# Performance work log

Measured on AMD Instinct MI355X. Metric: run time of the kernel, lower is better.

The kernel has to match this reference:

```python
import jax, jax.numpy as jnp
import numpy as np

D_MODEL = 1024
N_HEADS = 16
HEAD_DIM = D_MODEL // N_HEADS
NEG = -10000.0  # module uses -10000, not -inf


def setup_inputs() -> dict:
    key = jax.random.key(0)
    ks = jax.random.split(key, 8)
    B, T = 4, 2048
    q = jax.random.normal(ks[0], (B, T, D_MODEL), dtype=jnp.float32)
    k = jax.random.normal(ks[1], (B, T, D_MODEL), dtype=jnp.float32)
    v = jax.random.normal(ks[2], (B, T, D_MODEL), dtype=jnp.float32)
    attn_mask = jnp.ones((B, T), dtype=jnp.float32)
    # xavier_uniform for square [d, d] weights: limit = sqrt(6/(d+d))
    lim = float(np.sqrt(6.0 / (D_MODEL + D_MODEL)))
    Wq = jax.random.uniform(ks[3], (D_MODEL, D_MODEL), jnp.float32, -lim, lim)
    Wk = jax.random.uniform(ks[4], (D_MODEL, D_MODEL), jnp.float32, -lim, lim)
    Wv = jax.random.uniform(ks[5], (D_MODEL, D_MODEL), jnp.float32, -lim, lim)
    Wo = jax.random.uniform(ks[6], (D_MODEL, D_MODEL), jnp.float32, -lim, lim)
    return {"q": q, "k": k, "v": v, "attn_mask": attn_mask,
            "Wq": Wq, "Wk": Wk, "Wv": Wv, "Wo": Wo, "mask_future": 1}


def _split_heads(x):
    B, T, _ = x.shape
    return x.reshape(B, T, N_HEADS, HEAD_DIM).transpose(0, 2, 1, 3)  # [B,H,T,D]


def reference(q, k, v, attn_mask, Wq, Wk, Wv, Wo, mask_future):
    # torch Linear: y = x @ W.T  (weights stored [out, in])
    qh = _split_heads(jnp.einsum('btd,ed->bte', q, Wq))
    kh = _split_heads(jnp.einsum('btd,ed->bte', k, Wk))
    vh = _split_heads(jnp.einsum('btd,ed->bte', v, Wv))
    L, S = qh.shape[-2], kh.shape[-2]
    # dual scale: each of q and k scaled by 1/d**0.25
    scale = 1.0 / jnp.sqrt(jnp.sqrt(jnp.float32(HEAD_DIM)))
    scores = jnp.einsum('bhld,bhsd->bhls', qh * scale, kh * scale)
    if mask_future:
        causal_bias = jnp.triu(jnp.full((L, S), NEG, dtype=scores.dtype), k=1)
        scores = scores + causal_bias
    # padding mask: attn_mask [B, S] -> broadcast [B,1,1,S]; 0 entries -> -10000
    pad = attn_mask[:, None, None, :]
    scores = jnp.where(pad == 0, jnp.asarray(NEG, scores.dtype), scores)
    probs = jax.nn.softmax(scores, axis=-1)  # dropout p=0.0 -> identity
    ctx = jnp.einsum('bhls,bhsd->bhld', probs, vh)
    B = ctx.shape[0]
    ctx = ctx.transpose(0, 2, 1, 3).reshape(B, L, D_MODEL)
    return jnp.einsum('btd,ed->bte', ctx, Wo)
```

## Files before the change

kernel.cpp:

```cpp
#include <hip/hip_runtime.h>

typedef unsigned short u16;
typedef __attribute__((ext_vector_type(8))) _Float16 f16x8;
typedef __attribute__((ext_vector_type(2))) __fp16 fp16v2;
typedef __attribute__((ext_vector_type(4))) float f32x4;
typedef __attribute__((ext_vector_type(16))) float f32x16;

#define T_SEQ 2048
#define NH 16
#define DH 64
#define DM 1024
#define NEG2 (-14426.95f)
#define QS2 (0.42466089f)

__device__ __forceinline__ unsigned pk2(float a, float b) {
  union { fp16v2 v; unsigned u; } c;
  c.v = __builtin_amdgcn_cvt_pkrtz(a, b);
  return c.u;
}
__device__ __forceinline__ u16 f2h(float a) {
  union { _Float16 h; u16 u; } c; c.h = (_Float16)a; return c.u;
}

__device__ __forceinline__ void async_load16(const void* g, void* l) {
  __builtin_amdgcn_global_load_lds(
      (const __attribute__((address_space(1))) unsigned int*)(g),
      (__attribute__((address_space(3))) unsigned int*)(l), 16, 0, 0);
}

__global__ __launch_bounds__(256) void convert_all(
    const float* __restrict__ q, const float* __restrict__ k, const float* __restrict__ v,
    const float* __restrict__ Wq, const float* __restrict__ Wk, const float* __restrict__ Wv,
    const float* __restrict__ Wo, u16* __restrict__ xb, u16* __restrict__ wb) {
  int blk = blockIdx.x;
  const float* src; u16* dst;
  if (blk < 12288) {
    int s = blk >> 12;
    src = (s == 0) ? q : (s == 1) ? k : v;
    dst = xb + (size_t)s * 8388608u;
    blk &= 4095;
  } else {
    int s = (blk - 12288) >> 9;
    src = (s == 0) ? Wq : (s == 1) ? Wk : (s == 2) ? Wv : Wo;
    dst = wb + (size_t)s * 1048576u;
    blk = (blk - 12288) & 511;
  }
  size_t base = (size_t)blk * 2048 + (size_t)threadIdx.x * 8;
  float4 a = *(const float4*)(src + base);
  float4 b2 = *(const float4*)(src + base + 4);
  uint4 st;
  st.x = pk2(a.x, a.y); st.y = pk2(a.z, a.w);
  st.z = pk2(b2.x, b2.y); st.w = pk2(b2.z, b2.w);
  *(uint4*)(dst + base) = st;
}

__global__ __launch_bounds__(256) void gemm_qkv(const u16* __restrict__ A,
                                                const u16* __restrict__ Wqb,
                                                const u16* __restrict__ Wkb,
                                                const u16* __restrict__ Wvb,
                                                u16* __restrict__ Qh, u16* __restrict__ Kh,
                                                u16* __restrict__ VTh) {
  __shared__ char lds[49152];
  const int tid = threadIdx.x;
  const int wid = tid >> 6, lane = tid & 63;
  const int l32 = lane & 31, lh = lane >> 5;
  const int m0 = blockIdx.x * 128;
  const int n0 = blockIdx.y * 128;
  const int which = n0 >> 10;
  const int n0l = n0 & 1023;
  const u16* As = A + (size_t)which * 8388608u;
  const u16* Bw = (which == 0) ? Wqb : (which == 1) ? Wkb : Wvb;
  const int wm = wid >> 1, wn = wid & 1;
  f32x16 acc[2][2] = {};

  const u16* gA = As + (size_t)(m0 + wid * 32 + l32) * 1024 + lh * 8;
  const u16* gB = Bw + (size_t)(n0l + wid * 32 + l32) * 1024 + lh * 8;
  for (int t = 0; t < 2; ++t) {
    char* bf = lds + t * 16384;
    async_load16(gA + t * 32, bf + (wid * 2 + 0) * 1024);
    async_load16(gA + t * 32 + 16, bf + (wid * 2 + 1) * 1024);
    async_load16(gB + t * 32, bf + 8192 + (wid * 2 + 0) * 1024);
    async_load16(gB + t * 32 + 16, bf + 8192 + (wid * 2 + 1) * 1024);
  }

  int buf = 0;
  for (int it = 0; it < 32; ++it) {
    if (it < 31) asm volatile("s_waitcnt vmcnt(4)" ::: "memory");
    else         asm volatile("s_waitcnt vmcnt(0)" ::: "memory");
    __builtin_amdgcn_s_barrier();
    asm volatile("" ::: "memory");
    char* cur = lds + buf * 16384;
    if (it < 30) {
      char* nxt = lds + ((buf == 0) ? 2 : buf - 1) * 16384;
      int kt = (it + 2) * 32;
      async_load16(gA + kt, nxt + (wid * 2 + 0) * 1024);
      async_load16(gA + kt + 16, nxt + (wid * 2 + 1) * 1024);
      async_load16(gB + kt, nxt + 8192 + (wid * 2 + 0) * 1024);
      async_load16(gB + kt + 16, nxt + 8192 + (wid * 2 + 1) * 1024);
    }
    char* const rb = (which < 2) ? (cur + 8192) : cur;
    char* const cb = (which < 2) ? cur : (cur + 8192);
    f16x8 rf0[2], cf0[2], rf1[2], cf1[2];
    for (int i = 0; i < 2; ++i) {
      rf0[i] = *(const f16x8*)(rb + ((wm * 2 + i) * 2 + 0) * 1024 + lane * 16);
      cf0[i] = *(const f16x8*)(cb + ((wn * 2 + i) * 2 + 0) * 1024 + lane * 16);
    }
    for (int i = 0; i < 2; ++i) {
      rf1[i] = *(const f16x8*)(rb + ((wm * 2 + i) * 2 + 1) * 1024 + lane * 16);
      cf1[i] = *(const f16x8*)(cb + ((wn * 2 + i) * 2 + 1) * 1024 + lane * 16);
    }
    for (int i = 0; i < 2; ++i)
      for (int j = 0; j < 2; ++j)
        acc[i][j] = __builtin_amdgcn_mfma_f32_32x32x16_f16(rf0[i], cf0[j], acc[i][j], 0, 0, 0);
    for (int i = 0; i < 2; ++i)
      for (int j = 0; j < 2; ++j)
        acc[i][j] = __builtin_amdgcn_mfma_f32_32x32x16_f16(rf1[i], cf1[j], acc[i][j], 0, 0, 0);
    buf = (buf == 2) ? 0 : buf + 1;
  }

  const float s = (which < 2) ? QS2 : 1.0f;
  __syncthreads();
  for (int i = 0; i < 2; ++i)
    for (int j = 0; j < 2; ++j) {
      int colb = wn * 64 + j * 32 + l32;
      int rowb = wm * 64 + i * 32 + 4 * lh;
      for (int g = 0; g < 4; ++g) {
        uint2 pv;
        pv.x = pk2(acc[i][j][4 * g + 0] * s, acc[i][j][4 * g + 1] * s);
        pv.y = pk2(acc[i][j][4 * g + 2] * s, acc[i][j][4 * g + 3] * s);
        *(uint2*)(lds + colb * 264 + (rowb + 8 * g) * 2) = pv;
      }
    }
  __syncthreads();

  const int b = m0 >> 11, t0 = m0 & 2047, h0 = n0l >> 6;
  if (which < 2) {
    u16* O = which ? Kh : Qh;
    for (int p = 0; p < 8; ++p) {
      int row = p * 16 + (tid >> 4);
      int seg = tid & 15;
      uint4 val = *(const uint4*)(lds + row * 264 + seg * 16);
      int hl = seg >> 3, dh0 = (seg & 7) * 8;
      *(uint4*)(O + (((size_t)(b * NH + h0 + hl) * T_SEQ + t0 + row) << 6) + dh0) = val;
    }
  } else {
    for (int p = 0; p < 8; ++p) {
      int row = p * 16 + (tid >> 4);
      int seg = tid & 15;
      uint4 val = *(const uint4*)(lds + row * 264 + seg * 16);
      int h = h0 + (row >> 6), dh = row & 63;
      *(uint4*)(VTh + (((size_t)(b * NH + h) * DH + dh) << 11) + t0 + seg * 8) = val;
    }
  }
}

__global__ __launch_bounds__(256) void gemm_out(const u16* __restrict__ A,
                                                const u16* __restrict__ Bw,
                                                float* __restrict__ O) {
  __shared__ char lds[49152];
  const int tid = threadIdx.x;
  const int wid = tid >> 6, lane = tid & 63;
  const int l32 = lane & 31, lh = lane >> 5;
  const int m0 = blockIdx.x * 128, n0 = blockIdx.y * 128;
  const int wm = wid >> 1, wn = wid & 1;
  f32x16 acc[2][2] = {};

  const u16* gA = A + (size_t)(m0 + wid * 32 + l32) * 1024 + lh * 8;
  const u16* gB = Bw + (size_t)(n0 + wid * 32 + l32) * 1024 + lh * 8;
  for (int t = 0; t < 2; ++t) {
    char* bf = lds + t * 16384;
    async_load16(gA + t * 32, bf + (wid * 2 + 0) * 1024);
    async_load16(gA + t * 32 + 16, bf + (wid * 2 + 1) * 1024);
    async_load16(gB + t * 32, bf + 8192 + (wid * 2 + 0) * 1024);
    async_load16(gB + t * 32 + 16, bf + 8192 + (wid * 2 + 1) * 1024);
  }

  int buf = 0;
  for (int it = 0; it < 32; ++it) {
    if (it < 31) asm volatile("s_waitcnt vmcnt(4)" ::: "memory");
    else         asm volatile("s_waitcnt vmcnt(0)" ::: "memory");
    __builtin_amdgcn_s_barrier();
    asm volatile("" ::: "memory");
    char* cur = lds + buf * 16384;
    if (it < 30) {
      char* nxt = lds + ((buf == 0) ? 2 : buf - 1) * 16384;
      int kt = (it + 2) * 32;
      async_load16(gA + kt, nxt + (wid * 2 + 0) * 1024);
      async_load16(gA + kt + 16, nxt + (wid * 2 + 1) * 1024);
      async_load16(gB + kt, nxt + 8192 + (wid * 2 + 0) * 1024);
      async_load16(gB + kt + 16, nxt + 8192 + (wid * 2 + 1) * 1024);
    }
    f16x8 af0[2], bf0[2], af1[2], bf1[2];
    for (int i = 0; i < 2; ++i) {
      af0[i] = *(const f16x8*)(cur + ((wm * 2 + i) * 2 + 0) * 1024 + lane * 16);
      bf0[i] = *(const f16x8*)(cur + 8192 + ((wn * 2 + i) * 2 + 0) * 1024 + lane * 16);
    }
    for (int i = 0; i < 2; ++i) {
      af1[i] = *(const f16x8*)(cur + ((wm * 2 + i) * 2 + 1) * 1024 + lane * 16);
      bf1[i] = *(const f16x8*)(cur + 8192 + ((wn * 2 + i) * 2 + 1) * 1024 + lane * 16);
    }
    for (int i = 0; i < 2; ++i)
      for (int j = 0; j < 2; ++j)
        acc[i][j] = __builtin_amdgcn_mfma_f32_32x32x16_f16(af0[i], bf0[j], acc[i][j], 0, 0, 0);
    for (int i = 0; i < 2; ++i)
      for (int j = 0; j < 2; ++j)
        acc[i][j] = __builtin_amdgcn_mfma_f32_32x32x16_f16(af1[i], bf1[j], acc[i][j], 0, 0, 0);
    buf = (buf == 2) ? 0 : buf + 1;
  }
  for (int i = 0; i < 2; ++i)
    for (int j = 0; j < 2; ++j) {
      int col = n0 + wn * 64 + j * 32 + l32;
      int rowb = m0 + wm * 64 + i * 32 + 4 * lh;
      for (int g = 0; g < 4; ++g)
        for (int rr = 0; rr < 4; ++rr)
          O[(size_t)(rowb + 8 * g + rr) * 1024 + col] = acc[i][j][4 * g + rr];
    }
}

__global__ __launch_bounds__(512) void attn_kernel(const u16* __restrict__ Qh,
                                                   const u16* __restrict__ Kh,
                                                   const u16* __restrict__ VTh,
                                                   const float* __restrict__ attn_mask,
                                                   const int* __restrict__ mfp,
                                                   u16* __restrict__ ctx) {
  __shared__ char kls[2][8192];
  __shared__ char vls[2][8192];
  __shared__ char pls[8][2048];
  __shared__ float maskb[T_SEQ];
  __shared__ int mzf;

  const int tid = threadIdx.x;
  const int wid = tid >> 6, lane = tid & 63;
  const int lm = lane & 15, lq = lane >> 4;
  const int bid = blockIdx.x;
  const int bh_i = bid & 63, p8 = bid >> 6;
  const int b = bh_i >> 4, h = bh_i & 15;
  const int mf = *mfp;
  const size_t bh = (size_t)(b * NH + h);
  const u16* Qbh = Qh + bh * T_SEQ * DH;
  const u16* Kbh = Kh + bh * T_SEQ * DH;
  const u16* VTbh = VTh + bh * DH * T_SEQ;

  if (tid == 0) mzf = 0;
  __syncthreads();
  {
    int az = 0;
    for (int i = tid; i < T_SEQ; i += 512) {
      float mv = attn_mask[(size_t)b * T_SEQ + i];
      maskb[i] = (mv == 0.0f) ? NEG2 : 0.0f;
      az |= (mv == 0.0f);
    }
    if (az) mzf = 1;
  }
  __syncthreads();
  const int maskzero = mzf;

  for (int half = 0; half < 2; ++half) {
    const int qt = half ? (15 - p8) : p8;
    const int q0 = qt * 128;
    const int qw = q0 + wid * 16;
    f16x8 qf[2];
    qf[0] = *(const f16x8*)(Qbh + (size_t)(qw + lm) * DH + lq * 8);
    qf[1] = *(const f16x8*)(Qbh + (size_t)(qw + lm) * DH + 32 + lq * 8);

    f32x4 acc[4] = {};
    float mprev = -1e30f, lsum = 0.f;

    const int nch = mf ? (qt + 1) * 2 : 32;
    __syncthreads();
    {
      async_load16(Kbh + (size_t)((wid >> 1) * 16 + lm) * DH + (wid & 1) * 32 + lq * 8,
                   kls[0] + wid * 1024);
      async_load16(VTbh + (size_t)((wid >> 1) * 16 + lm) * T_SEQ + (wid & 1) * 32 + lq * 8,
                   vls[0] + wid * 1024);
    }
    for (int c = 0; c < nch; ++c) {
      const int s0 = c * 64;
      asm volatile("s_waitcnt vmcnt(0)" ::: "memory");
      __builtin_amdgcn_s_barrier();
      asm volatile("" ::: "memory");
      if (c + 1 < nch) {
        const int s1 = s0 + 64;
        async_load16(Kbh + (size_t)(s1 + (wid >> 1) * 16 + lm) * DH + (wid & 1) * 32 + lq * 8,
                     kls[(c + 1) & 1] + wid * 1024);
        async_load16(VTbh + (size_t)((wid >> 1) * 16 + lm) * T_SEQ + s1 + (wid & 1) * 32 + lq * 8,
                     vls[(c + 1) & 1] + wid * 1024);
      }
      const char* kcur = kls[c & 1];
      const char* vcur = vls[c & 1];

      f32x4 sc[4];
      for (int st = 0; st < 4; ++st) {
        f32x4 z = {0.f, 0.f, 0.f, 0.f};
        sc[st] = z;
        for (int kk = 0; kk < 2; ++kk) {
          f16x8 kf = *(const f16x8*)(kcur + ((st * 2 + kk) * 64 + lane) * 16);
          sc[st] = __builtin_amdgcn_mfma_f32_16x16x32_f16(kf, qf[kk], sc[st], 0, 0, 0);
        }
      }
      if (maskzero) {
        for (int st = 0; st < 4; ++st) {
          f32x4 mb = *(const f32x4*)(maskb + s0 + st * 16 + lq * 4);
          for (int r = 0; r < 4; ++r) sc[st][r] += mb[r];
        }
      }
      if (mf && (s0 + 64 > qw)) {
        int qg = qw + lm;
        for (int st = 0; st < 4; ++st)
          for (int r = 0; r < 4; ++r)
            if (s0 + st * 16 + lq * 4 + r > qg) sc[st][r] = NEG2;
      }
      float mx = fmaxf(fmaxf(sc[0][0], sc[0][1]), fmaxf(sc[0][2], sc[0][3]));
      for (int st = 1; st < 4; ++st) {
        float t2 = fmaxf(fmaxf(sc[st][0], sc[st][1]), fmaxf(sc[st][2], sc[st][3]));
        mx = fmaxf(mx, t2);
      }
      mx = fmaxf(mx, __shfl_xor(mx, 16));
      mx = fmaxf(mx, __shfl_xor(mx, 32));
      float mn = mprev;
      if (__ballot(mx > mprev) != 0ull) {
        mn = fmaxf(mprev, mx);
        float alpha = exp2f(mprev - mn);
        for (int r = 0; r < 4; ++r) {
          float ar = __shfl(alpha, lq * 4 + r);
          for (int nt = 0; nt < 4; ++nt) acc[nt][r] *= ar;
        }
        lsum *= alpha;
        mprev = mn;
      }
      float ps = 0.f;
      for (int st = 0; st < 4; ++st)
        for (int r = 0; r < 4; ++r) {
          float p = exp2f(sc[st][r] - mn);
          sc[st][r] = p;
          ps += p;
        }
      ps += __shfl_xor(ps, 16);
      ps += __shfl_xor(ps, 32);
      lsum += ps;
      {
        char* pw = pls[wid];
        for (int st = 0; st < 4; ++st) {
          int kk = st >> 1;
          int lqp = (st & 1) * 2 + (lq >> 1);
          uint2 pv;
          pv.x = pk2(sc[st][0], sc[st][1]);
          pv.y = pk2(sc[st][2], sc[st][3]);
          *(uint2*)(pw + kk * 1024 + (lqp * 16 + lm) * 16 + (lq & 1) * 8) = pv;
        }
      }
      asm volatile("s_waitcnt lgkmcnt(0)" ::: "memory");
      for (int kk = 0; kk < 2; ++kk) {
        f16x8 pf = *(const f16x8*)(pls[wid] + kk * 1024 + lane * 16);
        for (int nt = 0; nt < 4; ++nt) {
          f16x8 vf = *(const f16x8*)(vcur + ((nt * 2 + kk) * 64 + lane) * 16);
          acc[nt] = __builtin_amdgcn_mfma_f32_16x16x32_f16(pf, vf, acc[nt], 0, 0, 0);
        }
      }
    }
    float inv = 1.0f / lsum;
    for (int r = 0; r < 4; ++r) {
      float ir = __shfl(inv, lq * 4 + r);
      int t = qw + lq * 4 + r;
      for (int nt = 0; nt < 4; ++nt)
        ctx[((size_t)(b * T_SEQ + t) * DM) + h * DH + nt * 16 + lm] = f2h(acc[nt][r] * ir);
    }
  }
}

extern "C" void kernel_launch(void* const* d_in, const int* in_sizes, int n_in,
                              void* d_out, int out_size, void* d_ws, size_t ws_size,
                              hipStream_t stream) {
  const float* q = (const float*)d_in[0];
  const float* k = (const float*)d_in[1];
  const float* v = (const float*)d_in[2];
  const float* attn_mask = (const float*)d_in[3];
  const float* Wq = (const float*)d_in[4];
  const float* Wk = (const float*)d_in[5];
  const float* Wv = (const float*)d_in[6];
  const float* Wo = (const float*)d_in[7];
  const int* mf = (const int*)d_in[8];

  u16* ws = (u16*)d_ws;
  u16* qb  = ws;
  u16* wqb = ws + 3u * 8388608u;
  u16* wkb = wqb + 1048576u;
  u16* wvb = wkb + 1048576u;
  u16* wob = wvb + 1048576u;
  u16* Qh  = wob + 1048576u;
  u16* Kh  = Qh + 8388608u;
  u16* VTh = Kh + 8388608u;
  u16* ctxb = ws;

  convert_all<<<14336, 256, 0, stream>>>(q, k, v, Wq, Wk, Wv, Wo, qb, wqb);

  dim3 gq(64, 24);
  gemm_qkv<<<gq, 256, 0, stream>>>(qb, wqb, wkb, wvb, Qh, Kh, VTh);

  attn_kernel<<<512, 512, 0, stream>>>(Qh, Kh, VTh, attn_mask, mf, ctxb);

  dim3 gg(64, 8);
  gemm_out<<<gg, 256, 0, stream>>>(ctxb, wob, (float*)d_out);
}
```

Measured before the change: 370.7 us.

## Enlarge QKV GEMM tile to 256x128 with 8 waves and phased pipeline

Result: faster. 359.5 us (-3.0%).

```diff
diff --git a/kernel.cpp b/kernel.cpp
--- a/kernel.cpp
+++ b/kernel.cpp
@@ -54,27 +54,174 @@
   *(uint4*)(dst + base) = st;
 }
 
-__global__ __launch_bounds__(256) void gemm_qkv(const u16* __restrict__ A,
+__global__ __launch_bounds__(512) void gemm_qkv(const u16* __restrict__ A,
                                                 const u16* __restrict__ Wqb,
                                                 const u16* __restrict__ Wkb,
                                                 const u16* __restrict__ Wvb,
                                                 u16* __restrict__ Qh, u16* __restrict__ Kh,
                                                 u16* __restrict__ VTh) {
-  __shared__ char lds[49152];
+  __shared__ char lds[147456];
   const int tid = threadIdx.x;
   const int wid = tid >> 6, lane = tid & 63;
   const int l32 = lane & 31, lh = lane >> 5;
-  const int m0 = blockIdx.x * 128;
+  const int m0 = blockIdx.x * 256;
   const int n0 = blockIdx.y * 128;
   const int which = n0 >> 10;
   const int n0l = n0 & 1023;
   const u16* As = A + (size_t)which * 8388608u;
   const u16* Bw = (which == 0) ? Wqb : (which == 1) ? Wkb : Wvb;
+  f32x16 acc[2][2] = {};
+
+  const u16* gsrc[6]; int ldso[6];
+#pragma unroll
+  for (int u = 0; u < 6; ++u) {
+    int c = wid * 6 + u;
+    ldso[u] = c * 1024;
+    if (c < 32)
+      gsrc[u] = As + (size_t)(m0 + (c >> 2) * 32 + l32) * 1024 + (c & 3) * 16 + lh * 8;
+    else {
+      int cw = c - 32;
+      gsrc[u] = Bw + (size_t)(n0l + (cw >> 2) * 32 + l32) * 1024 + (cw & 3) * 16 + lh * 8;
+    }
+  }
+
+  const int rOff = (which < 2) ? 32768 : 0;
+  const int cOff = 32768 - rOff;
+  const int rgo = (which < 2) ? ((wid & 1) * 2) : ((wid >> 1) * 2);
+  const int cgo = (which < 2) ? ((wid >> 1) * 2) : ((wid & 1) * 2);
+
+#pragma unroll
+  for (int u = 0; u < 6; ++u) async_load16(gsrc[u] + 0 * 64, lds + 0 * 49152 + ldso[u]);
+#pragma unroll
+  for (int u = 0; u < 6; ++u) async_load16(gsrc[u] + 1 * 64, lds + 1 * 49152 + ldso[u]);
+  asm volatile("s_waitcnt vmcnt(6)" ::: "memory");
+  __builtin_amdgcn_s_barrier();
+  asm volatile("" ::: "memory");
+
+  int slotc = 0, slotn = 2;
+  for (int kt = 0; kt < 16; ++kt) {
+    char* bufc = lds + slotc * 49152;
+    char* bufn = lds + slotn * 49152;
+    const char* rb = bufc + rOff;
+    const char* cb = bufc + cOff;
+    f16x8 a0[4], a1[4], b0[4], b1[4];
+#pragma unroll
+    for (int k = 0; k < 4; ++k) {
+      a0[k] = *(const f16x8*)(rb + ((rgo + 0) * 4 + k) * 1024 + lane * 16);
+      b0[k] = *(const f16x8*)(cb + ((cgo + 0) * 4 + k) * 1024 + lane * 16);
+      b1[k] = *(const f16x8*)(cb + ((cgo + 1) * 4 + k) * 1024 + lane * 16);
+    }
+    if (kt < 14) {
+#pragma unroll
+      for (int u = 0; u < 3; ++u) async_load16(gsrc[u] + (kt + 2) * 64, bufn + ldso[u]);
+    }
+    asm volatile("" ::: "memory");
+    __builtin_amdgcn_s_barrier();
+    asm volatile("s_waitcnt lgkmcnt(0)" ::: "memory");
+    __builtin_amdgcn_sched_barrier(0);
+    __builtin_amdgcn_s_setprio(1);
+#pragma unroll
+    for (int k = 0; k < 4; ++k) {
+      acc[0][0] = __builtin_amdgcn_mfma_f32_32x32x16_f16(a0[k], b0[k], acc[0][0], 0, 0, 0);
+      acc[0][1] = __builtin_amdgcn_mfma_f32_32x32x16_f16(a0[k], b1[k], acc[0][1], 0, 0, 0);
+    }
+    __builtin_amdgcn_s_setprio(0);
+    asm volatile("" ::: "memory");
+    __builtin_amdgcn_s_barrier();
+#pragma unroll
+    for (int k = 0; k < 4; ++k)
+      a1[k] = *(const f16x8*)(rb + ((rgo + 1) * 4 + k) * 1024 + lane * 16);
+    if (kt < 14) {
+#pragma unroll
+      for (int u = 3; u < 6; ++u) async_load16(gsrc[u] + (kt + 2) * 64, bufn + ldso[u]);
+    }
+    if (kt < 14) asm volatile("s_waitcnt vmcnt(6)" ::: "memory");
+    else         asm volatile("s_waitcnt vmcnt(0)" ::: "memory");
+    asm volatile("" ::: "memory");
+    __builtin_amdgcn_s_barrier();
+    asm volatile("s_waitcnt lgkmcnt(0)" ::: "memory");
+    __builtin_amdgcn_sched_barrier(0);
+    __builtin_amdgcn_s_setprio(1);
+#pragma unroll
+    for (int k = 0; k < 4; ++k) {
+      acc[1][0] = __builtin_amdgcn_mfma_f32_32x32x16_f16(a1[k], b0[k], acc[1][0], 0, 0, 0);
+      acc[1][1] = __builtin_amdgcn_mfma_f32_32x32x16_f16(a1[k], b1[k], acc[1][1], 0, 0, 0);
+    }
+    __builtin_amdgcn_s_setprio(0);
+    asm volatile("" ::: "memory");
+    __builtin_amdgcn_s_barrier();
+    slotc = (slotc == 2) ? 0 : slotc + 1;
+    slotn = (slotn == 2) ? 0 : slotn + 1;
+  }
+
+  const float s = (which < 2) ? QS2 : 1.0f;
+  const int b = m0 >> 11, t0 = m0 & 2047, h0 = n0l >> 6;
+  __syncthreads();
+  if (which < 2) {
+#pragma unroll
+    for (int i = 0; i < 2; ++i)
+#pragma unroll
+      for (int j = 0; j < 2; ++j) {
+        int colb = (wid >> 1) * 64 + j * 32 + l32;
+        int rowb = (wid & 1) * 64 + i * 32 + 4 * lh;
+#pragma unroll
+        for (int g = 0; g < 4; ++g) {
+          uint2 pv;
+          pv.x = pk2(acc[i][j][4 * g + 0] * s, acc[i][j][4 * g + 1] * s);
+          pv.y = pk2(acc[i][j][4 * g + 2] * s, acc[i][j][4 * g + 3] * s);
+          *(uint2*)(lds + colb * 264 + (rowb + 8 * g) * 2) = pv;
+        }
+      }
+    __syncthreads();
+    u16* O = which ? Kh : Qh;
+#pragma unroll
+    for (int p = 0; p < 8; ++p) {
+      int row = p * 32 + (tid >> 4);
+      int seg = tid & 15;
+      uint4 val = *(const uint4*)(lds + row * 264 + seg * 16);
+      int hl = seg >> 3, dh0 = (seg & 7) * 8;
+      *(uint4*)(O + (((size_t)(b * NH + h0 + hl) * T_SEQ + t0 + row) << 6) + dh0) = val;
+    }
+  } else {
+#pragma unroll
+    for (int i = 0; i < 2; ++i)
+#pragma unroll
+      for (int j = 0; j < 2; ++j) {
+        int colb = (wid & 1) * 64 + j * 32 + l32;
+        int rowb = (wid >> 1) * 64 + i * 32 + 4 * lh;
+#pragma unroll
+        for (int g = 0; g < 4; ++g) {
+          uint2 pv;
+          pv.x = pk2(acc[i][j][4 * g + 0], acc[i][j][4 * g + 1]);
+          pv.y = pk2(acc[i][j][4 * g + 2], acc[i][j][4 * g + 3]);
+          *(uint2*)(lds + colb * 520 + (rowb + 8 * g) * 2) = pv;
+        }
+      }
+    __syncthreads();
+#pragma unroll
+    for (int p = 0; p < 8; ++p) {
+      int row = p * 16 + (tid >> 5);
+      int seg = tid & 31;
+      uint4 val = *(const uint4*)(lds + row * 520 + seg * 16);
+      int h = h0 + (row >> 6), dh = row & 63;
+      *(uint4*)(VTh + (((size_t)(b * NH + h) * DH + dh) << 11) + t0 + seg * 8) = val;
+    }
+  }
+}
+
+__global__ __launch_bounds__(256) void gemm_out(const u16* __restrict__ A,
+                                                const u16* __restrict__ Bw,
+                                                float* __restrict__ O) {
+  __shared__ char lds[49152];
+  const int tid = threadIdx.x;
+  const int wid = tid >> 6, lane = tid & 63;
+  const int l32 = lane & 31, lh = lane >> 5;
+  const int m0 = blockIdx.x * 128, n0 = blockIdx.y * 128;
   const int wm = wid >> 1, wn = wid & 1;
   f32x16 acc[2][2] = {};
 
-  const u16* gA = As + (size_t)(m0 + wid * 32 + l32) * 1024 + lh * 8;
-  const u16* gB = Bw + (size_t)(n0l + wid * 32 + l32) * 1024 + lh * 8;
+  const u16* gA = A + (size_t)(m0 + wid * 32 + l32) * 1024 + lh * 8;
+  const u16* gB = Bw + (size_t)(n0 + wid * 32 + l32) * 1024 + lh * 8;
   for (int t = 0; t < 2; ++t) {
     char* bf = lds + t * 16384;
     async_load16(gA + t * 32, bf + (wid * 2 + 0) * 1024);
@@ -98,98 +245,6 @@
       async_load16(gB + kt, nxt + 8192 + (wid * 2 + 0) * 1024);
       async_load16(gB + kt + 16, nxt + 8192 + (wid * 2 + 1) * 1024);
     }
-    char* const rb = (which < 2) ? (cur + 8192) : cur;
-    char* const cb = (which < 2) ? cur : (cur + 8192);
-    f16x8 rf0[2], cf0[2], rf1[2], cf1[2];
-    for (int i = 0; i < 2; ++i) {
-      rf0[i] = *(const f16x8*)(rb + ((wm * 2 + i) * 2 + 0) * 1024 + lane * 16);
-      cf0[i] = *(const f16x8*)(cb + ((wn * 2 + i) * 2 + 0) * 1024 + lane * 16);
-    }
-    for (int i = 0; i < 2; ++i) {
-      rf1[i] = *(const f16x8*)(rb + ((wm * 2 + i) * 2 + 1) * 1024 + lane * 16);
-      cf1[i] = *(const f16x8*)(cb + ((wn * 2 + i) * 2 + 1) * 1024 + lane * 16);
-    }
-    for (int i = 0; i < 2; ++i)
-      for (int j = 0; j < 2; ++j)
-        acc[i][j] = __builtin_amdgcn_mfma_f32_32x32x16_f16(rf0[i], cf0[j], acc[i][j], 0, 0, 0);
-    for (int i = 0; i < 2; ++i)
-      for (int j = 0; j < 2; ++j)
-        acc[i][j] = __builtin_amdgcn_mfma_f32_32x32x16_f16(rf1[i], cf1[j], acc[i][j], 0, 0, 0);
-    buf = (buf == 2) ? 0 : buf + 1;
-  }
-
-  const float s = (which < 2) ? QS2 : 1.0f;
-  __syncthreads();
-  for (int i = 0; i < 2; ++i)
-    for (int j = 0; j < 2; ++j) {
-      int colb = wn * 64 + j * 32 + l32;
-      int rowb = wm * 64 + i * 32 + 4 * lh;
-      for (int g = 0; g < 4; ++g) {
-        uint2 pv;
-        pv.x = pk2(acc[i][j][4 * g + 0] * s, acc[i][j][4 * g + 1] * s);
-        pv.y = pk2(acc[i][j][4 * g + 2] * s, acc[i][j][4 * g + 3] * s);
-        *(uint2*)(lds + colb * 264 + (rowb + 8 * g) * 2) = pv;
-      }
-    }
-  __syncthreads();
-
-  const int b = m0 >> 11, t0 = m0 & 2047, h0 = n0l >> 6;
-  if (which < 2) {
-    u16* O = which ? Kh : Qh;
-    for (int p = 0; p < 8; ++p) {
-      int row = p * 16 + (tid >> 4);
-      int seg = tid & 15;
-      uint4 val = *(const uint4*)(lds + row * 264 + seg * 16);
-      int hl = seg >> 3, dh0 = (seg & 7) * 8;
-      *(uint4*)(O + (((size_t)(b * NH + h0 + hl) * T_SEQ + t0 + row) << 6) + dh0) = val;
-    }
-  } else {
-    for (int p = 0; p < 8; ++p) {
-      int row = p * 16 + (tid >> 4);
-      int seg = tid & 15;
-      uint4 val = *(const uint4*)(lds + row * 264 + seg * 16);
-      int h = h0 + (row >> 6), dh = row & 63;
-      *(uint4*)(VTh + (((size_t)(b * NH + h) * DH + dh) << 11) + t0 + seg * 8) = val;
-    }
-  }
-}
-
-__global__ __launch_bounds__(256) void gemm_out(const u16* __restrict__ A,
-                                                const u16* __restrict__ Bw,
-                                                float* __restrict__ O) {
-  __shared__ char lds[49152];
-  const int tid = threadIdx.x;
-  const int wid = tid >> 6, lane = tid & 63;
-  const int l32 = lane & 31, lh = lane >> 5;
-  const int m0 = blockIdx.x * 128, n0 = blockIdx.y * 128;
-  const int wm = wid >> 1, wn = wid & 1;
-  f32x16 acc[2][2] = {};
-
-  const u16* gA = A + (size_t)(m0 + wid * 32 + l32) * 1024 + lh * 8;
-  const u16* gB = Bw + (size_t)(n0 + wid * 32 + l32) * 1024 + lh * 8;
-  for (int t = 0; t < 2; ++t) {
-    char* bf = lds + t * 16384;
-    async_load16(gA + t * 32, bf + (wid * 2 + 0) * 1024);
-    async_load16(gA + t * 32 + 16, bf + (wid * 2 + 1) * 1024);
-    async_load16(gB + t * 32, bf + 8192 + (wid * 2 + 0) * 1024);
-    async_load16(gB + t * 32 + 16, bf + 8192 + (wid * 2 + 1) * 1024);
-  }
-
-  int buf = 0;
-  for (int it = 0; it < 32; ++it) {
-    if (it < 31) asm volatile("s_waitcnt vmcnt(4)" ::: "memory");
-    else         asm volatile("s_waitcnt vmcnt(0)" ::: "memory");
-    __builtin_amdgcn_s_barrier();
-    asm volatile("" ::: "memory");
-    char* cur = lds + buf * 16384;
-    if (it < 30) {
-      char* nxt = lds + ((buf == 0) ? 2 : buf - 1) * 16384;
-      int kt = (it + 2) * 32;
-      async_load16(gA + kt, nxt + (wid * 2 + 0) * 1024);
-      async_load16(gA + kt + 16, nxt + (wid * 2 + 1) * 1024);
-      async_load16(gB + kt, nxt + 8192 + (wid * 2 + 0) * 1024);
-      async_load16(gB + kt + 16, nxt + 8192 + (wid * 2 + 1) * 1024);
-    }
     f16x8 af0[2], bf0[2], af1[2], bf1[2];
     for (int i = 0; i < 2; ++i) {
       af0[i] = *(const f16x8*)(cur + ((wm * 2 + i) * 2 + 0) * 1024 + lane * 16);
@@ -394,8 +449,8 @@
 
   convert_all<<<14336, 256, 0, stream>>>(q, k, v, Wq, Wk, Wv, Wo, qb, wqb);
 
-  dim3 gq(64, 24);
-  gemm_qkv<<<gq, 256, 0, stream>>>(qb, wqb, wkb, wvb, Qh, Kh, VTh);
+  dim3 gq(32, 24);
+  gemm_qkv<<<gq, 512, 0, stream>>>(qb, wqb, wkb, wvb, Qh, Kh, VTh);
 
   attn_kernel<<<512, 512, 0, stream>>>(Qh, Kh, VTh, attn_mask, mf, ctxb);
 
```
